# Optimization experiments

Measured on AMD Instinct MI355X. Metric: run time of the kernel, lower is better.

The kernel has to match this reference:

```python
import jax, jax.numpy as jnp
import numpy as np

N_NODES = 4096
N_EDGES = 131072
F_DIM = 16
H_DIM = 32

def _mlp_params(key, in_dim, hidden):
    ks = jax.random.split(key, 6)
    s1 = 1.0 / np.sqrt(in_dim); s2 = 1.0 / np.sqrt(hidden)
    return dict(
        W1=jax.random.uniform(ks[0], (in_dim, hidden), jnp.float32, -s1, s1),
        b1=jax.random.uniform(ks[1], (hidden,), jnp.float32, -s1, s1),
        W2=jax.random.uniform(ks[2], (hidden, hidden), jnp.float32, -s2, s2),
        b2=jax.random.uniform(ks[3], (hidden,), jnp.float32, -s2, s2),
        W3=jax.random.uniform(ks[4], (hidden, 1), jnp.float32, -s2, s2),
        b3=jax.random.uniform(ks[5], (1,), jnp.float32, -s2, s2),
    )

def _mlp(x, W1, b1, W2, b2, W3, b3):
    h = jax.nn.relu(x @ W1 + b1)
    h = jax.nn.relu(h @ W2 + b2)
    return (h @ W3 + b3)[..., 0]  # (E,)

def setup_inputs() -> dict:
    key = jax.random.key(0)
    k_ei, k_ef, k_s, k_p = jax.random.split(key, 4)
    edge_index = jax.random.randint(k_ei, (N_EDGES, 2), 0, N_NODES, dtype=jnp.int32)
    edge_feat = jax.random.normal(k_ef, (N_EDGES, F_DIM), dtype=jnp.float32)
    sh = _mlp_params(k_s, F_DIM, H_DIM)
    sp = _mlp_params(k_p, F_DIM, H_DIM)
    return dict(
        species_idx=0,
        edge_index=edge_index,
        edge_feat=edge_feat,
        num_nodes=N_NODES,
        sW1=sh['W1'], sb1=sh['b1'], sW2=sh['W2'], sb2=sh['b2'], sW3=sh['W3'], sb3=sh['b3'],
        pW1=sp['W1'], pb1=sp['b1'], pW2=sp['W2'], pb2=sp['b2'], pW3=sp['W3'], pb3=sp['b3'],
    )

def reference(species_idx, edge_index, edge_feat, num_nodes,
              sW1, sb1, sW2, sb2, sW3, sb3,
              pW1, pb1, pW2, pb2, pW3, pb3):
    # Edge logits: shared head + species head (species_idx selects the head;
    # here the selected head's params are passed directly).
    shared = _mlp(edge_feat, sW1, sb1, sW2, sb2, sW3, sb3)   # (E,)
    species = _mlp(edge_feat, pW1, pb1, pW2, pb2, pW3, pb3)  # (E,)
    resistance = jax.nn.softplus(shared + species) + 1e-4
    conductance = 1.0 / resistance
    i = edge_index[:, 0]
    j = edge_index[:, 1]
    # Scatter-assembled graph Laplacian (N x N)
    L = jnp.zeros((num_nodes, num_nodes), dtype=edge_feat.dtype)
    L = L.at[i, i].add(conductance)
    L = L.at[j, j].add(conductance)
    L = L.at[i, j].add(-conductance)
    L = L.at[j, i].add(-conductance)
    L_pinv = jnp.linalg.pinv(L)
    diag = jnp.diagonal(L_pinv)
    R = diag[:, None] + diag[None, :] - 2.0 * L_pinv
    return R, shared, species
```

## Files before the change

kernel.cpp:

```cpp
#include <hip/hip_runtime.h>
#include <hip/hip_bf16.h>


#define NN 4096
#define LDA 4096
#define NEDGE 131072
#define INVN (1.0f/4096.0f)

__device__ __forceinline__ float mlp_eval(const float* __restrict__ w,
                                          const float* __restrict__ x) {
  float h1[32], h2[32];
#pragma unroll
  for (int o = 0; o < 32; o += 4) {
    float4 s = *(const float4*)&w[512 + o];
#pragma unroll
    for (int i = 0; i < 16; ++i) {
      float4 wv = *(const float4*)&w[i * 32 + o];
      s.x = fmaf(x[i], wv.x, s.x); s.y = fmaf(x[i], wv.y, s.y);
      s.z = fmaf(x[i], wv.z, s.z); s.w = fmaf(x[i], wv.w, s.w);
    }
    h1[o] = fmaxf(s.x, 0.f); h1[o+1] = fmaxf(s.y, 0.f);
    h1[o+2] = fmaxf(s.z, 0.f); h1[o+3] = fmaxf(s.w, 0.f);
  }
#pragma unroll
  for (int o = 0; o < 32; o += 4) {
    float4 s = *(const float4*)&w[1568 + o];
#pragma unroll
    for (int i = 0; i < 32; ++i) {
      float4 wv = *(const float4*)&w[544 + i * 32 + o];
      s.x = fmaf(h1[i], wv.x, s.x); s.y = fmaf(h1[i], wv.y, s.y);
      s.z = fmaf(h1[i], wv.z, s.z); s.w = fmaf(h1[i], wv.w, s.w);
    }
    h2[o] = fmaxf(s.x, 0.f); h2[o+1] = fmaxf(s.y, 0.f);
    h2[o+2] = fmaxf(s.z, 0.f); h2[o+3] = fmaxf(s.w, 0.f);
  }
  float out = w[1632];
#pragma unroll
  for (int i = 0; i < 32; ++i) out = fmaf(h2[i], w[1600 + i], out);
  return out;
}

__global__ __launch_bounds__(256) void mlp_kernel(
    const float* __restrict__ ef,
    const float* __restrict__ sW1, const float* __restrict__ sb1,
    const float* __restrict__ sW2, const float* __restrict__ sb2,
    const float* __restrict__ sW3, const float* __restrict__ sb3,
    const float* __restrict__ pW1, const float* __restrict__ pb1,
    const float* __restrict__ pW2, const float* __restrict__ pb2,
    const float* __restrict__ pW3, const float* __restrict__ pb3,
    float* __restrict__ outS, float* __restrict__ outP,
    float* __restrict__ cond) {
  __shared__ float w[3328];
  int t = threadIdx.x;
  for (int i = t; i < 512; i += 256) { w[i] = sW1[i]; w[1664 + i] = pW1[i]; }
  for (int i = t; i < 1024; i += 256) { w[544 + i] = sW2[i]; w[1664 + 544 + i] = pW2[i]; }
  if (t < 32) {
    w[512 + t] = sb1[t]; w[1568 + t] = sb2[t]; w[1600 + t] = sW3[t];
    w[1664 + 512 + t] = pb1[t]; w[1664 + 1568 + t] = pb2[t]; w[1664 + 1600 + t] = pW3[t];
  }
  if (t == 0) { w[1632] = sb3[0]; w[1664 + 1632] = pb3[0]; }
  __syncthreads();
  int e = blockIdx.x * 256 + t;
  float x[16];
#pragma unroll
  for (int i = 0; i < 16; i += 4) {
    float4 v = *(const float4*)&ef[(size_t)e * 16 + i];
    x[i] = v.x; x[i+1] = v.y; x[i+2] = v.z; x[i+3] = v.w;
  }
  float s = mlp_eval(w, x);
  float p = mlp_eval(w + 1664, x);
  outS[e] = s; outP[e] = p;
  float z = s + p;
  float sp = fmaxf(z, 0.f) + log1pf(expf(-fabsf(z)));
  cond[e] = 1.0f / (sp + 1e-4f);
}

__global__ __launch_bounds__(256) void init_A(float* __restrict__ A) {
  size_t q = (size_t)blockIdx.x * 256 + threadIdx.x;
  *(float4*)&A[q * 4] = make_float4(INVN, INVN, INVN, INVN);
}

__global__ __launch_bounds__(256) void scatter_kernel(const int* __restrict__ ei,
                                                      const float* __restrict__ cond,
                                                      float* __restrict__ A) {
  int e = blockIdx.x * 256 + threadIdx.x;
  int i = ei[2 * e], j = ei[2 * e + 1];
  float c = cond[e];
  atomicAdd(&A[(size_t)i * (LDA + 1)], c);
  atomicAdd(&A[(size_t)j * (LDA + 1)], c);
  atomicAdd(&A[(size_t)i * LDA + j], -c);
  atomicAdd(&A[(size_t)j * LDA + i], -c);
}

__device__ __forceinline__ float rlane(float v, int l) {
  return __int_as_float(__builtin_amdgcn_readlane(__float_as_int(v), l));
}

__global__ __launch_bounds__(64) void potf2_wave(float* __restrict__ A, int k,
                                                 float* __restrict__ GinvAll) {
  float* blk = A + (size_t)k * 64 * (LDA + 1);
  const int lane = threadIdx.x;
  float a[64], x[64];
#pragma unroll
  for (int c = 0; c < 64; c += 4) {
    float4 v = *(const float4*)&blk[(size_t)lane * LDA + c];
    a[c] = v.x; a[c+1] = v.y; a[c+2] = v.z; a[c+3] = v.w;
    x[c]   = (c   == lane) ? 1.f : 0.f;
    x[c+1] = (c+1 == lane) ? 1.f : 0.f;
    x[c+2] = (c+2 == lane) ? 1.f : 0.f;
    x[c+3] = (c+3 == lane) ? 1.f : 0.f;
  }
#pragma unroll
  for (int j = 0; j < 64; ++j) {
    float dj = rlane(a[j], j);
    float inv = 1.0f / sqrtf(dj);
    float lij = a[j] * inv;
    a[j] = lij;
    float coefT = -lij;
    float sX = (lane == j) ? inv : 1.0f;
    float coefX = (lane > j) ? -lij : 0.0f;
#pragma unroll
    for (int c = j + 1; c < 64; ++c)
      a[c] = fmaf(coefT, rlane(lij, c), a[c]);
#pragma unroll
    for (int c = 0; c <= j; ++c) {
      float xjc = rlane(x[c], j) * inv;
      x[c] = fmaf(coefX, xjc, x[c] * sX);
    }
  }
  float* Gk = GinvAll + (size_t)k * 4096;
#pragma unroll
  for (int c = 0; c < 64; c += 4) {
    *(float4*)&blk[(size_t)lane * LDA + c] = make_float4(a[c], a[c+1], a[c+2], a[c+3]);
    *(float4*)&Gk[lane * 64 + c] = make_float4(x[c], x[c+1], x[c+2], x[c+3]);
  }
}

template <bool TA, bool TB, bool ACCUM, bool LOWER, bool KST, bool CCOMP>
__global__ __launch_bounds__(256) void gemm64(
    const float* __restrict__ Ab, long long aZ, int lda,
    const float* __restrict__ Bb, long long bZ, int ldb,
    float* __restrict__ Cb, long long cZ, int ldc, int K, float alpha) {
  int ti = blockIdx.x, tj = blockIdx.y;
  if (LOWER && tj > ti) return;
  const float* A = Ab + (long long)blockIdx.z * aZ;
  const float* B = Bb + (long long)blockIdx.z * bZ;
  __shared__ float As[16][68], Bs[16][68];
  int tid = threadIdx.x;
  int tx = tid & 15, ty = tid >> 4;
  float acc[4][4] = {};
  int m0 = ti * 64, n0 = tj * 64;
  int k0 = KST ? ti * 64 : 0;
  for (int k = k0; k < K; k += 16) {
    if (!TA) {
      int r = tid >> 2, c4 = (tid & 3) * 4;
      float4 v = *(const float4*)&A[(size_t)(m0 + r) * lda + k + c4];
      As[c4 + 0][r] = v.x; As[c4 + 1][r] = v.y; As[c4 + 2][r] = v.z; As[c4 + 3][r] = v.w;
    } else {
      int r = tid >> 4, c4 = (tid & 15) * 4;
      *(float4*)&As[r][c4] = *(const float4*)&A[(size_t)(k + r) * lda + m0 + c4];
    }
    if (TB) {
      int r = tid >> 2, c4 = (tid & 3) * 4;
      float4 v = *(const float4*)&B[(size_t)(n0 + r) * ldb + k + c4];
      Bs[c4 + 0][r] = v.x; Bs[c4 + 1][r] = v.y; Bs[c4 + 2][r] = v.z; Bs[c4 + 3][r] = v.w;
    } else {
      int r = tid >> 4, c4 = (tid & 15) * 4;
      *(float4*)&Bs[r][c4] = *(const float4*)&B[(size_t)(k + r) * ldb + n0 + c4];
    }
    __syncthreads();
#pragma unroll
    for (int kk = 0; kk < 16; ++kk) {
      float4 av = *(const float4*)&As[kk][ty * 4];
      float4 bv = *(const float4*)&Bs[kk][tx * 4];
      float a[4] = {av.x, av.y, av.z, av.w};
      float b[4] = {bv.x, bv.y, bv.z, bv.w};
#pragma unroll
      for (int i = 0; i < 4; ++i)
#pragma unroll
        for (int jj = 0; jj < 4; ++jj) acc[i][jj] = fmaf(a[i], b[jj], acc[i][jj]);
    }
    __syncthreads();
  }
  if (CCOMP) {
    float* C = Cb + ((size_t)ti * (ti + 1) / 2 + tj) * 4096;
#pragma unroll
    for (int i = 0; i < 4; ++i) {
      float4 c;
      c.x = alpha * acc[i][0]; c.y = alpha * acc[i][1];
      c.z = alpha * acc[i][2]; c.w = alpha * acc[i][3];
      *(float4*)&C[(ty * 4 + i) * 64 + tx * 4] = c;
    }
  } else {
    float* C = Cb + (long long)blockIdx.z * cZ;
#pragma unroll
    for (int i = 0; i < 4; ++i) {
      size_t off = (size_t)(m0 + ty * 4 + i) * ldc + n0 + tx * 4;
      float4 c;
      if (ACCUM) {
        c = *(float4*)&C[off];
        c.x += alpha * acc[i][0]; c.y += alpha * acc[i][1];
        c.z += alpha * acc[i][2]; c.w += alpha * acc[i][3];
      } else {
        c.x = alpha * acc[i][0]; c.y = alpha * acc[i][1];
        c.z = alpha * acc[i][2]; c.w = alpha * acc[i][3];
      }
      *(float4*)&C[off] = c;
    }
  }
}

template <bool TA, bool TB, bool ACCUM, bool TRI, bool KST, bool CCOMP>
__global__ __launch_bounds__(256) void gemm128(
    const float* __restrict__ Ab, long long aZ, int lda,
    const float* __restrict__ Bb, long long bZ, int ldb,
    float* __restrict__ Cb, long long cZ, int ldc, int K, float alpha) {
  int ti, tj;
  if (TRI) {
    int bid = blockIdx.x;
    ti = (int)((sqrtf(8.0f * bid + 1.0f) - 1.0f) * 0.5f);
    while ((ti + 1) * (ti + 2) / 2 <= bid) ++ti;
    while (ti * (ti + 1) / 2 > bid) --ti;
    tj = bid - ti * (ti + 1) / 2;
  } else {
    ti = blockIdx.x; tj = blockIdx.y;
  }
  const float* A = Ab + (long long)blockIdx.z * aZ;
  const float* B = Bb + (long long)blockIdx.z * bZ;
  __shared__ float As[16][132], Bs[16][132];
  int tid = threadIdx.x;
  int tx = tid & 15, ty = tid >> 4;
  float acc[8][8] = {};
  int m0 = ti * 128, n0 = tj * 128;
  int k0 = KST ? ti * 128 : 0;
  for (int k = k0; k < K; k += 16) {
    if (!TA) {
      int r = tid >> 1, c8 = (tid & 1) * 8;
      const float* src = &A[(size_t)(m0 + r) * lda + k + c8];
      float4 v0 = *(const float4*)src;
      float4 v1 = *(const float4*)(src + 4);
      As[c8 + 0][r] = v0.x; As[c8 + 1][r] = v0.y; As[c8 + 2][r] = v0.z; As[c8 + 3][r] = v0.w;
      As[c8 + 4][r] = v1.x; As[c8 + 5][r] = v1.y; As[c8 + 6][r] = v1.z; As[c8 + 7][r] = v1.w;
    } else {
      int r = tid >> 4, c8 = (tid & 15) * 8;
      const float* src = &A[(size_t)(k + r) * lda + m0 + c8];
      *(float4*)&As[r][c8]     = *(const float4*)src;
      *(float4*)&As[r][c8 + 4] = *(const float4*)(src + 4);
    }
    if (TB) {
      int r = tid >> 1, c8 = (tid & 1) * 8;
      const float* src = &B[(size_t)(n0 + r) * ldb + k + c8];
      float4 v0 = *(const float4*)src;
      float4 v1 = *(const float4*)(src + 4);
      Bs[c8 + 0][r] = v0.x; Bs[c8 + 1][r] = v0.y; Bs[c8 + 2][r] = v0.z; Bs[c8 + 3][r] = v0.w;
      Bs[c8 + 4][r] = v1.x; Bs[c8 + 5][r] = v1.y; Bs[c8 + 6][r] = v1.z; Bs[c8 + 7][r] = v1.w;
    } else {
      int r = tid >> 4, c8 = (tid & 15) * 8;
      const float* src = &B[(size_t)(k + r) * ldb + n0 + c8];
      *(float4*)&Bs[r][c8]     = *(const float4*)src;
      *(float4*)&Bs[r][c8 + 4] = *(const float4*)(src + 4);
    }
    __syncthreads();
#pragma unroll
    for (int kk = 0; kk < 16; ++kk) {
      float a8[8], b8[8];
      *(float4*)&a8[0] = *(const float4*)&As[kk][ty * 4];
      *(float4*)&a8[4] = *(const float4*)&As[kk][64 + ty * 4];
      *(float4*)&b8[0] = *(const float4*)&Bs[kk][tx * 4];
      *(float4*)&b8[4] = *(const float4*)&Bs[kk][64 + tx * 4];
#pragma unroll
      for (int i = 0; i < 8; ++i)
#pragma unroll
        for (int jj = 0; jj < 8; ++jj) acc[i][jj] = fmaf(a8[i], b8[jj], acc[i][jj]);
    }
    __syncthreads();
  }
  if (CCOMP) {
#pragma unroll
    for (int hr = 0; hr < 2; ++hr) {
      int TI = 2 * ti + hr;
#pragma unroll
      for (int hc = 0; hc < 2; ++hc) {
        int TJ = 2 * tj + hc;
        if (TJ > TI) continue;
        float* C = Cb + ((size_t)TI * (TI + 1) / 2 + TJ) * 4096;
#pragma unroll
        for (int i = 0; i < 4; ++i) {
          float4 c;
          c.x = alpha * acc[hr * 4 + i][hc * 4 + 0];
          c.y = alpha * acc[hr * 4 + i][hc * 4 + 1];
          c.z = alpha * acc[hr * 4 + i][hc * 4 + 2];
          c.w = alpha * acc[hr * 4 + i][hc * 4 + 3];
          *(float4*)&C[(ty * 4 + i) * 64 + tx * 4] = c;
        }
      }
    }
  } else {
    float* C = Cb + (long long)blockIdx.z * cZ;
#pragma unroll
    for (int i = 0; i < 8; ++i) {
      int row = (i < 4) ? (m0 + ty * 4 + i) : (m0 + 64 + ty * 4 + i - 4);
      float* dst0 = &C[(size_t)row * ldc + n0 + tx * 4];
      float* dst1 = dst0 + 64;
      float4 c0, c1;
      c0.x = alpha * acc[i][0]; c0.y = alpha * acc[i][1];
      c0.z = alpha * acc[i][2]; c0.w = alpha * acc[i][3];
      c1.x = alpha * acc[i][4]; c1.y = alpha * acc[i][5];
      c1.z = alpha * acc[i][6]; c1.w = alpha * acc[i][7];
      if (ACCUM) {
        float4 o0 = *(float4*)dst0, o1 = *(float4*)dst1;
        c0.x += o0.x; c0.y += o0.y; c0.z += o0.z; c0.w += o0.w;
        c1.x += o1.x; c1.y += o1.y; c1.z += o1.z; c1.w += o1.w;
      }
      *(float4*)dst0 = c0;
      *(float4*)dst1 = c1;
    }
  }
}

__global__ __launch_bounds__(256) void finish_W_prep(float* __restrict__ A,
                                                     const float* __restrict__ GinvAll) {
  size_t q = (size_t)blockIdx.x * 256 + threadIdx.x;
  int r = (int)(q >> 10), c4 = (int)(q & 1023) << 2;
  int rb = r >> 6, cb = c4 >> 6;
  if (cb == rb) {
    const float* g = GinvAll + (size_t)rb * 4096 + (size_t)(r & 63) * 64 + (c4 & 63);
    *(float4*)&A[q * 4] = *(const float4*)g;
  } else if (cb > rb) {
    *(float4*)&A[q * 4] = make_float4(0.f, 0.f, 0.f, 0.f);
  }
}

__global__ __launch_bounds__(256) void copy_diag(const float* __restrict__ Mc,
                                                 float* __restrict__ d) {
  int i = blockIdx.x * 256 + threadIdx.x;
  int tb = i >> 6;
  size_t q = (size_t)tb * (tb + 1) / 2 + tb;
  d[i] = Mc[q * 4096 + (size_t)(i & 63) * 65];
}

__global__ __launch_bounds__(256) void final_R(const float* __restrict__ Mc,
                                               const float* __restrict__ d,
                                               float* __restrict__ out) {
  size_t idx = (size_t)blockIdx.x * 256 + threadIdx.x;
  int r = (int)(idx >> 12), c = (int)(idx & 4095);
  int a = r > c ? r : c, b = r > c ? c : r;
  int ta = a >> 6, tb = b >> 6;
  size_t q = (size_t)ta * (ta + 1) / 2 + tb;
  float m = Mc[q * 4096 + (size_t)(a & 63) * 64 + (b & 63)];
  out[idx] = d[r] + d[c] - 2.0f * m;
}

extern "C" void kernel_launch(void* const* d_in, const int* in_sizes, int n_in,
                              void* d_out, int out_size, void* d_ws, size_t ws_size,
                              hipStream_t stream) {
  const int* eidx = (const int*)d_in[1];
  const float* ef = (const float*)d_in[2];
  const float* sW1 = (const float*)d_in[4],  *sb1 = (const float*)d_in[5];
  const float* sW2 = (const float*)d_in[6],  *sb2 = (const float*)d_in[7];
  const float* sW3 = (const float*)d_in[8],  *sb3 = (const float*)d_in[9];
  const float* pW1 = (const float*)d_in[10], *pb1 = (const float*)d_in[11];
  const float* pW2 = (const float*)d_in[12], *pb2 = (const float*)d_in[13];
  const float* pW3 = (const float*)d_in[14], *pb3 = (const float*)d_in[15];

  float* dout = (float*)d_out;
  float* dA = dout;
  float* outS = dout + (size_t)NN * NN;
  float* outP = outS + NEDGE;

  float* ws = (float*)d_ws;
  float* Mc = ws;
  float* U = ws + 8519680ull;
  float* cond = U;
  float* Ginv = U;
  float* Tbuf = U;
  float* diagb = U;

  mlp_kernel<<<NEDGE / 256, 256, 0, stream>>>(ef, sW1, sb1, sW2, sb2, sW3, sb3,
                                              pW1, pb1, pW2, pb2, pW3, pb3,
                                              outS, outP, cond);
  init_A<<<(NN * NN / 4) / 256, 256, 0, stream>>>(dA);
  scatter_kernel<<<NEDGE / 256, 256, 0, stream>>>(eidx, cond, dA);

  for (int p = 0; p < 16; ++p) {
    int ct = p * 4;
    for (int kk = 0; kk < 4; ++kk) {
      int k = ct + kk;
      potf2_wave<<<1, 64, 0, stream>>>(dA, k, Ginv);
      int rem = NN - (k + 1) * 64;
      if (rem > 0) {
        float* panel = dA + (size_t)(k + 1) * 64 * LDA + (size_t)k * 64;
        gemm64<false, true, false, false, false, false>
            <<<dim3(rem / 64, 1, 1), 256, 0, stream>>>(
                panel, 0, LDA, Ginv + (size_t)k * 4096, 0, 64, panel, 0, LDA,
                64, 1.0f);
        int pcols = 3 - kk;
        if (pcols > 0) {
          float* trail = dA + (size_t)(k + 1) * 64 * (LDA + 1);
          gemm64<false, true, true, true, false, false>
              <<<dim3(rem / 64, pcols, 1), 256, 0, stream>>>(
                  panel, 0, LDA, panel, 0, LDA, trail, 0, LDA, 64, -1.0f);
        }
      }
    }
    int c0 = p * 256;
    int rem2 = NN - c0 - 256;
    if (rem2 > 0) {
      float* Lp = dA + (size_t)(c0 + 256) * LDA + c0;
      float* trail = dA + (size_t)(c0 + 256) * (LDA + 1);
      int nt = rem2 / 128;
      gemm128<false, true, true, true, false, false>
          <<<dim3(nt * (nt + 1) / 2, 1, 1), 256, 0, stream>>>(
              Lp, 0, LDA, Lp, 0, LDA, trail, 0, LDA, 256, -1.0f);
    }
  }

  finish_W_prep<<<(NN * NN / 4) / 256, 256, 0, stream>>>(dA, Ginv);

  for (int S = 64; S <= 2048; S *= 2) {
    int np = NN / (2 * S);
    long long pz = (long long)2 * S * (LDA + 1);
    if (S == 64) {
      gemm64<false, false, false, false, false, false>
          <<<dim3(1, 1, np), 256, 0, stream>>>(
              dA + (size_t)S * LDA, pz, LDA, dA, pz, LDA,
              Tbuf, (long long)S * S, S, S, 1.0f);
      gemm64<false, false, false, false, false, false>
          <<<dim3(1, 1, np), 256, 0, stream>>>(
              dA + (size_t)S * (LDA + 1), pz, LDA, Tbuf, (long long)S * S, S,
              dA + (size_t)S * LDA, pz, LDA, S, -1.0f);
    } else {
      gemm128<false, false, false, false, false, false>
          <<<dim3(S / 128, S / 128, np), 256, 0, stream>>>(
              dA + (size_t)S * LDA, pz, LDA, dA, pz, LDA,
              Tbuf, (long long)S * S, S, S, 1.0f);
      gemm128<false, false, false, false, false, false>
          <<<dim3(S / 128, S / 128, np), 256, 0, stream>>>(
              dA + (size_t)S * (LDA + 1), pz, LDA, Tbuf, (long long)S * S, S,
              dA + (size_t)S * LDA, pz, LDA, S, -1.0f);
    }
  }

  gemm128<true, false, false, true, true, true>
      <<<dim3(528, 1, 1), 256, 0, stream>>>(dA, 0, LDA, dA, 0, LDA, Mc, 0, 64,
                                            NN, 1.0f);

  copy_diag<<<NN / 256, 256, 0, stream>>>(Mc, diagb);
  final_R<<<(NN * NN) / 256, 256, 0, stream>>>(Mc, diagb, dout);
}
```

Before: 5.171 ms.

## Replace panel inverse with direct TRSM, exploit triangular K ranges, split-K final product

```diff
diff --git a/kernel.cpp b/kernel.cpp
--- a/kernel.cpp
+++ b/kernel.cpp
@@ -80,6 +80,11 @@
   *(float4*)&A[q * 4] = make_float4(INVN, INVN, INVN, INVN);
 }
 
+__global__ __launch_bounds__(256) void zero_ws(float* __restrict__ P) {
+  size_t q = (size_t)blockIdx.x * 256 + threadIdx.x;
+  *(float4*)&P[q * 4] = make_float4(0.f, 0.f, 0.f, 0.f);
+}
+
 __global__ __launch_bounds__(256) void scatter_kernel(const int* __restrict__ ei,
                                                       const float* __restrict__ cond,
                                                       float* __restrict__ A) {
@@ -96,19 +101,14 @@
   return __int_as_float(__builtin_amdgcn_readlane(__float_as_int(v), l));
 }
 
-__global__ __launch_bounds__(64) void potf2_wave(float* __restrict__ A, int k,
-                                                 float* __restrict__ GinvAll) {
+__global__ __launch_bounds__(64) void potf2_slim(float* __restrict__ A, int k) {
   float* blk = A + (size_t)k * 64 * (LDA + 1);
   const int lane = threadIdx.x;
-  float a[64], x[64];
+  float a[64];
 #pragma unroll
   for (int c = 0; c < 64; c += 4) {
     float4 v = *(const float4*)&blk[(size_t)lane * LDA + c];
     a[c] = v.x; a[c+1] = v.y; a[c+2] = v.z; a[c+3] = v.w;
-    x[c]   = (c   == lane) ? 1.f : 0.f;
-    x[c+1] = (c+1 == lane) ? 1.f : 0.f;
-    x[c+2] = (c+2 == lane) ? 1.f : 0.f;
-    x[c+3] = (c+3 == lane) ? 1.f : 0.f;
   }
 #pragma unroll
   for (int j = 0; j < 64; ++j) {
@@ -117,22 +117,83 @@
     float lij = a[j] * inv;
     a[j] = lij;
     float coefT = -lij;
-    float sX = (lane == j) ? inv : 1.0f;
-    float coefX = (lane > j) ? -lij : 0.0f;
 #pragma unroll
     for (int c = j + 1; c < 64; ++c)
       a[c] = fmaf(coefT, rlane(lij, c), a[c]);
-#pragma unroll
-    for (int c = 0; c <= j; ++c) {
-      float xjc = rlane(x[c], j) * inv;
-      x[c] = fmaf(coefX, xjc, x[c] * sX);
-    }
-  }
-  float* Gk = GinvAll + (size_t)k * 4096;
-#pragma unroll
-  for (int c = 0; c < 64; c += 4) {
+  }
+#pragma unroll
+  for (int c = 0; c < 64; c += 4)
     *(float4*)&blk[(size_t)lane * LDA + c] = make_float4(a[c], a[c+1], a[c+2], a[c+3]);
-    *(float4*)&Gk[lane * 64 + c] = make_float4(x[c], x[c+1], x[c+2], x[c+3]);
+}
+
+__global__ __launch_bounds__(256) void trsm_direct(float* __restrict__ A, int k) {
+  __shared__ float S[64][65], Ld[64][65], red[64][4];
+  __shared__ float invd[64];
+  int tid = threadIdx.x;
+  int r = tid & 63, part = tid >> 6;
+  int c0 = k * 64;
+  int r0 = c0 + 64 + blockIdx.x * 64;
+  for (int q = tid; q < 1024; q += 256) {
+    int rr = q >> 4, c4 = (q & 15) << 2;
+    *(float4*)&S[rr][c4] = *(const float4*)&A[(size_t)(r0 + rr) * LDA + c0 + c4];
+    *(float4*)&Ld[rr][c4] = *(const float4*)&A[(size_t)(c0 + rr) * LDA + c0 + c4];
+  }
+  __syncthreads();
+  if (tid < 64) invd[tid] = 1.0f / Ld[tid][tid];
+  __syncthreads();
+  int kb = part * 16;
+  for (int c = 0; c < 64; ++c) {
+    float s = 0.f;
+    int ke = (kb + 16 < c) ? kb + 16 : c;
+    for (int kk = kb; kk < ke; ++kk)
+      s = fmaf(S[r][kk], Ld[c][kk], s);
+    red[r][part] = s;
+    __syncthreads();
+    if (part == 0) {
+      float tot = (red[r][0] + red[r][1]) + (red[r][2] + red[r][3]);
+      S[r][c] = (S[r][c] - tot) * invd[c];
+    }
+    __syncthreads();
+  }
+  for (int q = tid; q < 1024; q += 256) {
+    int rr = q >> 4, c4 = (q & 15) << 2;
+    *(float4*)&A[(size_t)(r0 + rr) * LDA + c0 + c4] = *(float4*)&S[rr][c4];
+  }
+}
+
+__global__ __launch_bounds__(256) void ginv_all(const float* __restrict__ A,
+                                                float* __restrict__ GinvAll) {
+  __shared__ float Ld[64][65], X[64][65], red[4][64];
+  __shared__ float invd[64];
+  int tid = threadIdx.x;
+  int c = tid & 63, part = tid >> 6;
+  int k = blockIdx.x;
+  const float* blk = A + (size_t)k * 64 * (LDA + 1);
+  for (int q = tid; q < 1024; q += 256) {
+    int rr = q >> 4, c4 = (q & 15) << 2;
+    *(float4*)&Ld[rr][c4] = *(const float4*)&blk[(size_t)rr * LDA + c4];
+  }
+  __syncthreads();
+  if (tid < 64) invd[tid] = 1.0f / Ld[tid][tid];
+  __syncthreads();
+  int kb = part * 16;
+  for (int i = 0; i < 64; ++i) {
+    float s = 0.f;
+    int ke = (kb + 16 < i) ? kb + 16 : i;
+    for (int kk = kb; kk < ke; ++kk)
+      s = fmaf(Ld[i][kk], X[kk][c], s);
+    red[part][c] = s;
+    __syncthreads();
+    if (part == 0) {
+      float tot = (red[0][c] + red[1][c]) + (red[2][c] + red[3][c]);
+      X[i][c] = ((i == c ? 1.f : 0.f) - tot) * invd[i];
+    }
+    __syncthreads();
+  }
+  float* G = GinvAll + (size_t)k * 4096;
+  for (int q = tid; q < 1024; q += 256) {
+    int rr = q >> 4, c4 = (q & 15) << 2;
+    *(float4*)&G[rr * 64 + c4] = *(float4*)&X[rr][c4];
   }
 }
 
@@ -182,35 +243,32 @@
     }
     __syncthreads();
   }
-  if (CCOMP) {
-    float* C = Cb + ((size_t)ti * (ti + 1) / 2 + tj) * 4096;
-#pragma unroll
-    for (int i = 0; i < 4; ++i) {
-      float4 c;
+  float* C = Cb + (long long)blockIdx.z * cZ;
+#pragma unroll
+  for (int i = 0; i < 4; ++i) {
+    size_t off = (size_t)(m0 + ty * 4 + i) * ldc + n0 + tx * 4;
+    float4 c;
+    if (ACCUM) {
+      c = *(float4*)&C[off];
+      c.x += alpha * acc[i][0]; c.y += alpha * acc[i][1];
+      c.z += alpha * acc[i][2]; c.w += alpha * acc[i][3];
+    } else {
       c.x = alpha * acc[i][0]; c.y = alpha * acc[i][1];
       c.z = alpha * acc[i][2]; c.w = alpha * acc[i][3];
-      *(float4*)&C[(ty * 4 + i) * 64 + tx * 4] = c;
-    }
-  } else {
-    float* C = Cb + (long long)blockIdx.z * cZ;
-#pragma unroll
-    for (int i = 0; i < 4; ++i) {
-      size_t off = (size_t)(m0 + ty * 4 + i) * ldc + n0 + tx * 4;
-      float4 c;
-      if (ACCUM) {
-        c = *(float4*)&C[off];
-        c.x += alpha * acc[i][0]; c.y += alpha * acc[i][1];
-        c.z += alpha * acc[i][2]; c.w += alpha * acc[i][3];
-      } else {
-        c.x = alpha * acc[i][0]; c.y = alpha * acc[i][1];
-        c.z = alpha * acc[i][2]; c.w = alpha * acc[i][3];
-      }
-      *(float4*)&C[off] = c;
-    }
-  }
-}
-
-template <bool TA, bool TB, bool ACCUM, bool TRI, bool KST, bool CCOMP>
+    }
+    *(float4*)&C[off] = c;
+  }
+}
+
+__device__ __forceinline__ int tri_i(int bid) {
+  int ti = (int)((sqrtf(8.0f * bid + 1.0f) - 1.0f) * 0.5f);
+  while ((ti + 1) * (ti + 2) / 2 <= bid) ++ti;
+  while (ti * (ti + 1) / 2 > bid) --ti;
+  return ti;
+}
+
+template <bool TA, bool TB, bool ACCUM, bool TRI, int KMODE, bool CCOMP,
+          bool ATOMIC, bool KSPLIT>
 __global__ __launch_bounds__(256) void gemm128(
     const float* __restrict__ Ab, long long aZ, int lda,
     const float* __restrict__ Bb, long long bZ, int ldb,
@@ -218,22 +276,26 @@
   int ti, tj;
   if (TRI) {
     int bid = blockIdx.x;
-    ti = (int)((sqrtf(8.0f * bid + 1.0f) - 1.0f) * 0.5f);
-    while ((ti + 1) * (ti + 2) / 2 <= bid) ++ti;
-    while (ti * (ti + 1) / 2 > bid) --ti;
+    ti = tri_i(bid);
     tj = bid - ti * (ti + 1) / 2;
   } else {
     ti = blockIdx.x; tj = blockIdx.y;
   }
-  const float* A = Ab + (long long)blockIdx.z * aZ;
-  const float* B = Bb + (long long)blockIdx.z * bZ;
+  int k0 = (KMODE == 1) ? ti * 128 : (KMODE == 2) ? tj * 128 : 0;
+  int kEnd = K;
+  if (KMODE == 3) { int ke = (ti + 1) * 128; kEnd = (ke < K) ? ke : K; }
+  if (KSPLIT) {
+    if (blockIdx.z == 0) { if (kEnd > 2048) kEnd = 2048; if (k0 >= kEnd) return; }
+    else { if (k0 < 2048) k0 = 2048; }
+  }
+  const float* A = KSPLIT ? Ab : Ab + (long long)blockIdx.z * aZ;
+  const float* B = KSPLIT ? Bb : Bb + (long long)blockIdx.z * bZ;
   __shared__ float As[16][132], Bs[16][132];
   int tid = threadIdx.x;
   int tx = tid & 15, ty = tid >> 4;
   float acc[8][8] = {};
   int m0 = ti * 128, n0 = tj * 128;
-  int k0 = KST ? ti * 128 : 0;
-  for (int k = k0; k < K; k += 16) {
+  for (int k = k0; k < kEnd; k += 16) {
     if (!TA) {
       int r = tid >> 1, c8 = (tid & 1) * 8;
       const float* src = &A[(size_t)(m0 + r) * lda + k + c8];
@@ -286,12 +348,20 @@
         float* C = Cb + ((size_t)TI * (TI + 1) / 2 + TJ) * 4096;
 #pragma unroll
         for (int i = 0; i < 4; ++i) {
-          float4 c;
-          c.x = alpha * acc[hr * 4 + i][hc * 4 + 0];
-          c.y = alpha * acc[hr * 4 + i][hc * 4 + 1];
-          c.z = alpha * acc[hr * 4 + i][hc * 4 + 2];
-          c.w = alpha * acc[hr * 4 + i][hc * 4 + 3];
-          *(float4*)&C[(ty * 4 + i) * 64 + tx * 4] = c;
+          if (ATOMIC) {
+            float* pbase = &C[(ty * 4 + i) * 64 + tx * 4];
+            atomicAdd(pbase + 0, alpha * acc[hr * 4 + i][hc * 4 + 0]);
+            atomicAdd(pbase + 1, alpha * acc[hr * 4 + i][hc * 4 + 1]);
+            atomicAdd(pbase + 2, alpha * acc[hr * 4 + i][hc * 4 + 2]);
+            atomicAdd(pbase + 3, alpha * acc[hr * 4 + i][hc * 4 + 3]);
+          } else {
+            float4 c;
+            c.x = alpha * acc[hr * 4 + i][hc * 4 + 0];
+            c.y = alpha * acc[hr * 4 + i][hc * 4 + 1];
+            c.z = alpha * acc[hr * 4 + i][hc * 4 + 2];
+            c.w = alpha * acc[hr * 4 + i][hc * 4 + 3];
+            *(float4*)&C[(ty * 4 + i) * 64 + tx * 4] = c;
+          }
         }
       }
     }
@@ -379,6 +449,7 @@
   mlp_kernel<<<NEDGE / 256, 256, 0, stream>>>(ef, sW1, sb1, sW2, sb2, sW3, sb3,
                                               pW1, pb1, pW2, pb2, pW3, pb3,
                                               outS, outP, cond);
+  zero_ws<<<2080, 256, 0, stream>>>(Mc);
   init_A<<<(NN * NN / 4) / 256, 256, 0, stream>>>(dA);
   scatter_kernel<<<NEDGE / 256, 256, 0, stream>>>(eidx, cond, dA);
 
@@ -386,16 +457,13 @@
     int ct = p * 4;
     for (int kk = 0; kk < 4; ++kk) {
       int k = ct + kk;
-      potf2_wave<<<1, 64, 0, stream>>>(dA, k, Ginv);
+      potf2_slim<<<1, 64, 0, stream>>>(dA, k);
       int rem = NN - (k + 1) * 64;
       if (rem > 0) {
-        float* panel = dA + (size_t)(k + 1) * 64 * LDA + (size_t)k * 64;
-        gemm64<false, true, false, false, false, false>
-            <<<dim3(rem / 64, 1, 1), 256, 0, stream>>>(
-                panel, 0, LDA, Ginv + (size_t)k * 4096, 0, 64, panel, 0, LDA,
-                64, 1.0f);
+        trsm_direct<<<rem / 64, 256, 0, stream>>>(dA, k);
         int pcols = 3 - kk;
         if (pcols > 0) {
+          float* panel = dA + (size_t)(k + 1) * 64 * LDA + (size_t)k * 64;
           float* trail = dA + (size_t)(k + 1) * 64 * (LDA + 1);
           gemm64<false, true, true, true, false, false>
               <<<dim3(rem / 64, pcols, 1), 256, 0, stream>>>(
@@ -409,12 +477,13 @@
       float* Lp = dA + (size_t)(c0 + 256) * LDA + c0;
       float* trail = dA + (size_t)(c0 + 256) * (LDA + 1);
       int nt = rem2 / 128;
-      gemm128<false, true, true, true, false, false>
+      gemm128<false, true, true, true, 0, false, false, false>
           <<<dim3(nt * (nt + 1) / 2, 1, 1), 256, 0, stream>>>(
               Lp, 0, LDA, Lp, 0, LDA, trail, 0, LDA, 256, -1.0f);
     }
   }
 
+  ginv_all<<<64, 256, 0, stream>>>(dA, Ginv);
   finish_W_prep<<<(NN * NN / 4) / 256, 256, 0, stream>>>(dA, Ginv);
 
   for (int S = 64; S <= 2048; S *= 2) {
@@ -430,19 +499,19 @@
               dA + (size_t)S * (LDA + 1), pz, LDA, Tbuf, (long long)S * S, S,
               dA + (size_t)S * LDA, pz, LDA, S, -1.0f);
     } else {
-      gemm128<false, false, false, false, false, false>
+      gemm128<false, false, false, false, 2, false, false, false>
           <<<dim3(S / 128, S / 128, np), 256, 0, stream>>>(
               dA + (size_t)S * LDA, pz, LDA, dA, pz, LDA,
               Tbuf, (long long)S * S, S, S, 1.0f);
-      gemm128<false, false, false, false, false, false>
+      gemm128<false, false, false, false, 3, false, false, false>
           <<<dim3(S / 128, S / 128, np), 256, 0, stream>>>(
               dA + (size_t)S * (LDA + 1), pz, LDA, Tbuf, (long long)S * S, S,
               dA + (size_t)S * LDA, pz, LDA, S, -1.0f);
     }
   }
 
-  gemm128<true, false, false, true, true, true>
-      <<<dim3(528, 1, 1), 256, 0, stream>>>(dA, 0, LDA, dA, 0, LDA, Mc, 0, 64,
+  gemm128<true, false, false, true, 1, true, true, true>
+      <<<dim3(528, 1, 2), 256, 0, stream>>>(dA, 0, LDA, dA, 0, LDA, Mc, 0, 64,
                                             NN, 1.0f);
 
   copy_diag<<<NN / 256, 256, 0, stream>>>(Mc, diagb);
```

New measurement: 7.211 ms. +39.4%, slower.
